# Optimization experiments

Hardware: AMD Instinct MI355X
Metric: run time of the kernel (lower is better)

Reference implementation:

```python
import jax, jax.numpy as jnp
import numpy as np

B, N, QD = 2, 2048, 1024
HEADS, DIM_HEAD = 16, 64
INNER = HEADS * DIM_HEAD  # 1024
SCALE = DIM_HEAD ** -0.5


def setup_inputs() -> dict:
    key = jax.random.key(0)
    ks = jax.random.split(key, 8)
    x = jax.random.normal(ks[0], (B, N, QD), dtype=jnp.float32)
    bias = jax.random.normal(ks[1], (B, N, N), dtype=jnp.float32)
    mask = jax.random.randint(ks[2], (B, N), 0, 2) > 0
    # parameters (nn.Linear stores weight [out, in]; we keep [in, out] and matmul x @ W)
    Wq = jax.random.normal(ks[3], (QD, INNER), dtype=jnp.float32) * (QD ** -0.5)
    Wkv = jax.random.normal(ks[4], (QD, 2 * INNER), dtype=jnp.float32) * (QD ** -0.5)
    Wo = jax.random.normal(ks[5], (INNER, QD), dtype=jnp.float32) * (INNER ** -0.5)
    bo = jax.random.normal(ks[6], (QD,), dtype=jnp.float32) * 0.01
    return {"x": x, "bias": bias, "mask": mask, "Wq": Wq, "Wkv": Wkv, "Wo": Wo, "bo": bo}


def reference(x, bias, mask, Wq, Wkv, Wo, bo):
    b, n, _ = x.shape
    q = x @ Wq                      # [b, n, inner]
    kv = x @ Wkv                    # [b, n, 2*inner] (context defaults to x)
    k, v = jnp.split(kv, 2, axis=-1)
    # split heads: [b, h, n, d]
    split = lambda t: t.reshape(b, n, HEADS, DIM_HEAD).transpose(0, 2, 1, 3)
    q, k, v = split(q), split(k), split(v)
    sim = jnp.einsum('bhid,bhjd->bhij', q, k) * SCALE   # [b, h, n, n]
    sim = sim + bias[:, None, :, :]                      # additive bias broadcast over heads
    max_neg = -jnp.finfo(sim.dtype).max
    sim = jnp.where(mask[:, None, None, :], sim, max_neg)  # per-key mask
    attn = jax.nn.softmax(sim, axis=-1)
    out = jnp.einsum('bhij,bhjd->bhid', attn, v)         # [b, h, n, d]
    out = out.transpose(0, 2, 1, 3).reshape(b, n, INNER)  # merge heads
    return out @ Wo + bo
```

## Files before the change

kernel.cpp:

```cpp
#include <hip/hip_runtime.h>
#include <hip/hip_bf16.h>
#include <stdint.h>

#define B_     2
#define N_     2048
#define QD_    1024
#define H_     16
#define DH_    64
#define INNER_ 1024
#define SCALE_ 0.125f

typedef unsigned short u16;
typedef __attribute__((ext_vector_type(8))) short bf16x8;
typedef __attribute__((ext_vector_type(4))) float f32x4;
typedef __attribute__((ext_vector_type(4))) unsigned short u16x4;
typedef __attribute__((ext_vector_type(8))) unsigned short u16x8;

__device__ inline u16 f2bf(float f) {
    union { float f; uint32_t u; } c; c.f = f;
    uint32_t r = c.u + 0x7FFFu + ((c.u >> 16) & 1u);
    return (u16)(r >> 16);
}
__device__ inline float bf2f(u16 s) {
    union { uint32_t u; float f; } c; c.u = ((uint32_t)s) << 16;
    return c.f;
}
__device__ inline void split2(float v, u16 &h, u16 &l) {
    u16 hs = f2bf(v);
    h = hs;
    l = f2bf(v - bf2f(hs));
}
__device__ inline unsigned pk2(float a, float b) {
    float2 f; f.x = a; f.y = b;
    union { __hip_bfloat162 v; unsigned u; } c;
    c.v = __float22bfloat162_rn(f);
    return c.u;
}

__global__ __launch_bounds__(256) void prep_kernel(
    const float* __restrict__ x, u16* __restrict__ xh, u16* __restrict__ xl,
    const float* __restrict__ Wq, const float* __restrict__ Wkv, const float* __restrict__ Wo,
    u16* __restrict__ wTh, u16* __restrict__ wTl,
    u16* __restrict__ woTh, u16* __restrict__ woTl)
{
    __shared__ float t[32][33];
    const int blk = blockIdx.x, tid = threadIdx.x;
    if (blk < 4096) {
        int idx = blk * 256 + tid;
        float4 v = ((const float4*)x)[idx];
        u16x4 hv, lv; u16 h, l;
        split2(v.x, h, l); hv.x = h; lv.x = l;
        split2(v.y, h, l); hv.y = h; lv.y = l;
        split2(v.z, h, l); hv.z = h; lv.z = l;
        split2(v.w, h, l); hv.w = h; lv.w = l;
        ((u16x4*)xh)[idx] = hv;
        ((u16x4*)xl)[idx] = lv;
        return;
    }
    int local = blk - 4096;
    const float* src; u16 *dhi, *dlo; int C, bx, by;
    if (local < 1024)      { src = Wq;  dhi = wTh;                dlo = wTl;                C = 1024; by = local >> 5; bx = local & 31; }
    else if (local < 3072) { int l2 = local - 1024; src = Wkv; dhi = wTh + 1024 * 1024; dlo = wTl + 1024 * 1024; C = 2048; by = l2 >> 6; bx = l2 & 63; }
    else                   { int l2 = local - 3072; src = Wo;  dhi = woTh;               dlo = woTl;               C = 1024; by = l2 >> 5; bx = l2 & 31; }
    const int x0 = bx * 32, y0 = by * 32;
    const int tx = tid & 31, ty = tid >> 5;
    for (int yy = ty; yy < 32; yy += 8)
        t[yy][tx] = src[(size_t)(y0 + yy) * C + x0 + tx];
    __syncthreads();
    for (int i = ty; i < 32; i += 8) {
        float v = t[tx][i];
        u16 h, l; split2(v, h, l);
        size_t o = (size_t)(x0 + i) * 1024 + y0 + tx;
        dhi[o] = h; dlo[o] = l;
    }
}

__global__ __launch_bounds__(256) void gemm_qkv_bias(
    int mode,
    const u16* __restrict__ Ah, const u16* __restrict__ Al,
    const u16* __restrict__ Bh,
    u16* __restrict__ qh,
    u16* __restrict__ kb, u16* __restrict__ vT,
    const float* __restrict__ bias, const int* __restrict__ mask,
    u16* __restrict__ bsw)
{
    __shared__ __align__(16) char smem[24576];
    const int tid = threadIdx.x;

    int gid = -1, bid = -1;
    if (mode == 1) {
        if (blockIdx.x < 768) gid = blockIdx.x; else bid = blockIdx.x - 768;
    } else if (mode == 0) gid = blockIdx.x;
    else bid = blockIdx.x;

    if (bid >= 0) {
        float (*t)[65] = (float(*)[65])smem;
        const int b = bid >> 10, rest = bid & 1023;
        const int k0 = (rest & 31) * 64, q0 = (rest >> 5) * 64;
#pragma unroll
        for (int it = 0; it < 16; it++) {
            int idx = it * 256 + tid;
            int qq = idx >> 6, kk = idx & 63;
            t[qq][kk] = bias[((size_t)b * N_ + q0 + qq) * N_ + k0 + kk];
        }
        __syncthreads();
        const u16 NEG = f2bf(-1e30f);
        const int qt = q0 >> 6, jt = k0 >> 7, w0 = (k0 >> 5) & 3;
        const int p = tid >> 1, hf = tid & 1;
        const int wv = w0 + (p >> 6), lane = p & 63;
        const int quad = lane >> 4, l16 = lane & 15;
        const int kbase = (p >> 6) * 32 + quad * 8 + hf * 4;
        const int4 mv = *(const int4*)&mask[b * N_ + k0 + kbase];
        const int mok[4] = { mv.x, mv.y, mv.z, mv.w };
        u16x8 o0, o1;
#pragma unroll
        for (int i = 0; i < 8; i++) {
            int m = i >> 2, r = i & 3;
            o0[i] = mok[r] ? f2bf(t[m * 16 + l16][kbase + r]) : NEG;
        }
#pragma unroll
        for (int i = 0; i < 8; i++) {
            int m = 2 + (i >> 2), r = i & 3;
            o1[i] = mok[r] ? f2bf(t[m * 16 + l16][kbase + r]) : NEG;
        }
        size_t ob = ((((size_t)b * 32 + qt) * 16 + jt) * 4 + wv) * 2048
                    + (size_t)lane * 32 + hf * 16;
        *(u16x8*)&bsw[ob]     = o0;
        *(u16x8*)&bsw[ob + 8] = o1;
        return;
    }

    u16* sAh = (u16*)smem;
    u16* sAl = (u16*)(smem + 8192);
    u16* sBh = (u16*)(smem + 16384);
    const int wave = tid >> 6, lane = tid & 63;
    const int quad = lane >> 4, l16 = lane & 15;
    const int wm = wave >> 1, wn = wave & 1;
    const int bx = gid % 24, by = gid / 24;
    const int bm = by * 128, bn = bx * 128;
    const bool comp = (bx < 8);

    f32x4 acc[4][4];
#pragma unroll
    for (int i = 0; i < 4; i++)
#pragma unroll
        for (int j = 0; j < 4; j++) acc[i][j] = (f32x4){0.f, 0.f, 0.f, 0.f};

    const int row0 = tid >> 2, g4 = tid & 3;
    const int r1 = row0, r2 = row0 + 64;
    const int gc1 = (g4 ^ (r1 & 3)) * 8, gc2 = (g4 ^ (r2 & 3)) * 8;
    const size_t a1 = (size_t)(bm + r1) * 1024 + gc1, a2 = (size_t)(bm + r2) * 1024 + gc2;
    const size_t b1 = (size_t)(bn + r1) * 1024 + gc1, b2 = (size_t)(bn + r2) * 1024 + gc2;
    const int w1 = r1 * 32 + g4 * 8, w2 = r2 * 32 + g4 * 8;

    bf16x8 pAh0, pAh1, pAl0, pAl1, pBh0, pBh1;
    pAh0 = *(const bf16x8*)&Ah[a1]; pAh1 = *(const bf16x8*)&Ah[a2];
    pBh0 = *(const bf16x8*)&Bh[b1]; pBh1 = *(const bf16x8*)&Bh[b2];
    if (comp) { pAl0 = *(const bf16x8*)&Al[a1]; pAl1 = *(const bf16x8*)&Al[a2]; }

    for (int k0 = 0; k0 < 1024; k0 += 32) {
        *(bf16x8*)&sAh[w1] = pAh0; *(bf16x8*)&sAh[w2] = pAh1;
        *(bf16x8*)&sBh[w1] = pBh0; *(bf16x8*)&sBh[w2] = pBh1;
        if (comp) { *(bf16x8*)&sAl[w1] = pAl0; *(bf16x8*)&sAl[w2] = pAl1; }
        __syncthreads();
        if (k0 + 32 < 1024) {
            int kn = k0 + 32;
            pAh0 = *(const bf16x8*)&Ah[a1 + kn]; pAh1 = *(const bf16x8*)&Ah[a2 + kn];
            pBh0 = *(const bf16x8*)&Bh[b1 + kn]; pBh1 = *(const bf16x8*)&Bh[b2 + kn];
            if (comp) { pAl0 = *(const bf16x8*)&Al[a1 + kn]; pAl1 = *(const bf16x8*)&Al[a2 + kn]; }
        }
        bf16x8 fah[4], fal[4], fbh[4];
#pragma unroll
        for (int s = 0; s < 4; s++) {
            int ra = wm * 64 + s * 16 + l16;
            int rb = wn * 64 + s * 16 + l16;
            int ca = (quad ^ (ra & 3)) * 8;
            int cb = (quad ^ (rb & 3)) * 8;
            fah[s] = *(const bf16x8*)&sAh[ra * 32 + ca];
            fbh[s] = *(const bf16x8*)&sBh[rb * 32 + cb];
            if (comp) fal[s] = *(const bf16x8*)&sAl[ra * 32 + ca];
        }
#pragma unroll
        for (int sm = 0; sm < 4; sm++)
#pragma unroll
            for (int sn = 0; sn < 4; sn++) {
                acc[sm][sn] = __builtin_amdgcn_mfma_f32_16x16x32_bf16(fah[sm], fbh[sn], acc[sm][sn], 0, 0, 0);
                if (comp)
                    acc[sm][sn] = __builtin_amdgcn_mfma_f32_16x16x32_bf16(fal[sm], fbh[sn], acc[sm][sn], 0, 0, 0);
            }
        __syncthreads();
    }
#pragma unroll
    for (int sm = 0; sm < 4; sm++) {
        int rowb = bm + wm * 64 + sm * 16 + quad * 4;
        int bb = rowb >> 11, i0 = rowb & 2047;
#pragma unroll
        for (int sn = 0; sn < 4; sn++) {
            int col = bn + wn * 64 + sn * 16 + l16;
            int region = col >> 10;
            int hh = (col >> 6) & 15;
            int d = col & 63;
            if (region == 0) {
#pragma unroll
                for (int r = 0; r < 4; r++) {
                    size_t o = (((size_t)(bb * H_ + hh)) * N_ + i0 + r) * DH_ + d;
                    qh[o] = f2bf(acc[sm][sn][r] * SCALE_);
                }
            } else if (region == 1) {
#pragma unroll
                for (int r = 0; r < 4; r++) {
                    size_t o = (((size_t)(bb * H_ + hh)) * N_ + i0 + r) * DH_ + d;
                    kb[o] = f2bf(acc[sm][sn][r]);
                }
            } else {
                u16x4 pv;
#pragma unroll
                for (int r = 0; r < 4; r++) pv[r] = f2bf(acc[sm][sn][r]);
                *(u16x4*)&vT[(((size_t)(bb * H_ + hh)) * DH_ + d) * N_ + i0] = pv;
            }
        }
    }
}

__global__ __launch_bounds__(256) void gemm_out(
    const u16* __restrict__ Ab,
    const u16* __restrict__ Bh,
    const float* __restrict__ bo, float* __restrict__ out)
{
    __shared__ __align__(16) u16 sA[128 * 32], sBh[64 * 32];
    const int tid = threadIdx.x;
    const int wave = tid >> 6, lane = tid & 63;
    const int quad = lane >> 4, l16 = lane & 15;
    const int wm = wave >> 1, wn = wave & 1;
    const int bm = blockIdx.y * 128, bn = blockIdx.x * 64;

    f32x4 acc[4][2];
#pragma unroll
    for (int i = 0; i < 4; i++)
#pragma unroll
        for (int j = 0; j < 2; j++) acc[i][j] = (f32x4){0.f, 0.f, 0.f, 0.f};

    const int row0 = tid >> 2, g4 = tid & 3;
    const int r1 = row0, r2 = row0 + 64;
    const int rb0 = tid >> 2;
    const int gc1 = (g4 ^ (r1 & 3)) * 8, gc2 = (g4 ^ (r2 & 3)) * 8;
    const size_t a1 = (size_t)(bm + r1) * 1024 + gc1, a2 = (size_t)(bm + r2) * 1024 + gc2;
    const size_t bgo = (size_t)(bn + rb0) * 1024 + gc1;
    const int w1 = r1 * 32 + g4 * 8, w2 = r2 * 32 + g4 * 8;
    const int wb = rb0 * 32 + g4 * 8;

    bf16x8 pA0, pA1, pBh0;
    pA0 = *(const bf16x8*)&Ab[a1]; pA1 = *(const bf16x8*)&Ab[a2];
    pBh0 = *(const bf16x8*)&Bh[bgo];

    for (int k0 = 0; k0 < 1024; k0 += 32) {
        *(bf16x8*)&sA[w1] = pA0;  *(bf16x8*)&sA[w2] = pA1;
        *(bf16x8*)&sBh[wb] = pBh0;
        __syncthreads();
        if (k0 + 32 < 1024) {
            int kn = k0 + 32;
            pA0 = *(const bf16x8*)&Ab[a1 + kn]; pA1 = *(const bf16x8*)&Ab[a2 + kn];
            pBh0 = *(const bf16x8*)&Bh[bgo + kn];
        }
        bf16x8 fa[4], fbh[2];
#pragma unroll
        for (int s = 0; s < 4; s++) {
            int ra = wm * 64 + s * 16 + l16;
            int ca = (quad ^ (ra & 3)) * 8;
            fa[s] = *(const bf16x8*)&sA[ra * 32 + ca];
        }
#pragma unroll
        for (int s = 0; s < 2; s++) {
            int rb = wn * 32 + s * 16 + l16;
            int cb = (quad ^ (rb & 3)) * 8;
            fbh[s] = *(const bf16x8*)&sBh[rb * 32 + cb];
        }
#pragma unroll
        for (int sm = 0; sm < 4; sm++)
#pragma unroll
            for (int sn = 0; sn < 2; sn++)
                acc[sm][sn] = __builtin_amdgcn_mfma_f32_16x16x32_bf16(fa[sm], fbh[sn], acc[sm][sn], 0, 0, 0);
        __syncthreads();
    }
#pragma unroll
    for (int sm = 0; sm < 4; sm++) {
        int rowb = bm + wm * 64 + sm * 16 + quad * 4;
#pragma unroll
        for (int sn = 0; sn < 2; sn++) {
            int col = bn + wn * 32 + sn * 16 + l16;
            float bv = bo[col];
#pragma unroll
            for (int r = 0; r < 4; r++)
                out[(size_t)(rowb + r) * 1024 + col] = acc[sm][sn][r] + bv;
        }
    }
}

#define LDK 72
#define LDV 128

__global__ __launch_bounds__(256, 2) void attn_kernel(
    const u16* __restrict__ qh,
    const u16* __restrict__ kb, const u16* __restrict__ vT,
    const u16* __restrict__ bsw, u16* __restrict__ ob)
{
    __shared__ __align__(16) char smem[35328];
    u16* sK  = (u16*)smem;
    u16* sVt = (u16*)(smem + 18432);
    float* rO = (float*)smem;
    float* rL = (float*)(smem + 34816);

    const int bh = blockIdx.y, b = bh >> 4, h = bh & 15;
    const int qt = blockIdx.x, qbase = qt * 64;
    const int tid = threadIdx.x, wave = tid >> 6, lane = tid & 63;
    const int quad = lane >> 4, l16 = lane & 15;

    bf16x8 aq[4][2];
#pragma unroll
    for (int m = 0; m < 4; m++) {
        size_t qo = ((size_t)bh * N_ + qbase + m * 16 + l16) * DH_ + quad * 8;
        aq[m][0] = *(const bf16x8*)&qh[qo];
        aq[m][1] = *(const bf16x8*)&qh[qo + 32];
    }
    f32x4 Oacc[4][4], lacc[4];
#pragma unroll
    for (int m = 0; m < 4; m++) {
        lacc[m] = (f32x4){0.f, 0.f, 0.f, 0.f};
#pragma unroll
        for (int nd = 0; nd < 4; nd++) Oacc[m][nd] = (f32x4){0.f, 0.f, 0.f, 0.f};
    }
    bf16x8 ones;
#pragma unroll
    for (int i = 0; i < 8; i++) ones[i] = (short)0x3F80;

    const int rK = tid >> 3, cK = (tid & 7) * 8;
    const int sigK = ((rK & 4) << 2) + ((rK >> 3) << 2) + (rK & 3);
    const int rV = tid >> 4;
    const int vg = tid & 15;
    const int cV = vg * 8;
    const int vsw = (vg ^ (rV & 7)) * 8;
    const int vrg = ((wave * 4 + quad) ^ (l16 & 7)) * 8;
    const size_t kgbase = (size_t)bh * N_ * DH_;
    const size_t vgbase = (size_t)bh * DH_ * N_;
    const size_t bswb = (size_t)(b * 32 + qt) * 131072 + (size_t)wave * 2048
                        + (size_t)lane * 32;

    bf16x8 pK[4], pV[4];
    u16x8 cB[4], nB[4];
#pragma unroll
    for (int it = 0; it < 4; it++) {
        pK[it] = *(const bf16x8*)&kb[kgbase + (size_t)(rK + it * 32) * DH_ + cK];
        pV[it] = *(const bf16x8*)&vT[vgbase + (size_t)(rV + it * 16) * N_ + cV];
    }
#pragma unroll
    for (int c = 0; c < 4; c++) cB[c] = *(const u16x8*)&bsw[bswb + c * 8];

    for (int jt = 0; jt < 16; jt++) {
#pragma unroll
        for (int it = 0; it < 4; it++) {
            *(bf16x8*)&sK[(it * 32 + sigK) * LDK + cK] = pK[it];
            *(bf16x8*)&sVt[(rV + it * 16) * LDV + vsw] = pV[it];
        }
        __syncthreads();
        {
            int jn = (jt + 1) & 15;
            int j0n = jn * 128;
#pragma unroll
            for (int it = 0; it < 4; it++) {
                pK[it] = *(const bf16x8*)&kb[kgbase + (size_t)(j0n + rK + it * 32) * DH_ + cK];
                pV[it] = *(const bf16x8*)&vT[vgbase + (size_t)(rV + it * 16) * N_ + j0n + cV];
            }
            size_t bb = bswb + (size_t)jn * 8192;
#pragma unroll
            for (int c = 0; c < 4; c++) nB[c] = *(const u16x8*)&bsw[bb + c * 8];
        }
        bf16x8 kf[2][2], vf[4];
#pragma unroll
        for (int n = 0; n < 2; n++)
#pragma unroll
            for (int s = 0; s < 2; s++)
                kf[n][s] = *(const bf16x8*)&sK[(wave * 32 + n * 16 + l16) * LDK + s * 32 + quad * 8];
#pragma unroll
        for (int nd = 0; nd < 4; nd++)
            vf[nd] = *(const bf16x8*)&sVt[(nd * 16 + l16) * LDV + vrg];

#pragma unroll
        for (int m = 0; m < 4; m++) {
            f32x4 S0 = (f32x4){0.f, 0.f, 0.f, 0.f};
            f32x4 S1 = (f32x4){0.f, 0.f, 0.f, 0.f};
#pragma unroll
            for (int s = 0; s < 2; s++) {
                S0 = __builtin_amdgcn_mfma_f32_16x16x32_bf16(kf[0][s], aq[m][s], S0, 0, 0, 0);
                S1 = __builtin_amdgcn_mfma_f32_16x16x32_bf16(kf[1][s], aq[m][s], S1, 0, 0, 0);
            }
            float p0[4], p1[4];
#pragma unroll
            for (int r = 0; r < 4; r++) {
                p0[r] = __expf(S0[r] + bf2f(cB[m >> 1][(m & 1) * 4 + r]));
                p1[r] = __expf(S1[r] + bf2f(cB[2 + (m >> 1)][(m & 1) * 4 + r]));
            }
            union { bf16x8 v; unsigned w[4]; } pa;
            pa.w[0] = pk2(p0[0], p0[1]);
            pa.w[1] = pk2(p0[2], p0[3]);
            pa.w[2] = pk2(p1[0], p1[1]);
            pa.w[3] = pk2(p1[2], p1[3]);
            lacc[m] = __builtin_amdgcn_mfma_f32_16x16x32_bf16(pa.v, ones, lacc[m], 0, 0, 0);
#pragma unroll
            for (int nd = 0; nd < 4; nd++)
                Oacc[m][nd] = __builtin_amdgcn_mfma_f32_16x16x32_bf16(pa.v, vf[nd], Oacc[m][nd], 0, 0, 0);
        }
#pragma unroll
        for (int c = 0; c < 4; c++) cB[c] = nB[c];
        __syncthreads();
    }

    if (wave >= 2) {
        int slot = wave - 2;
#pragma unroll
        for (int m = 0; m < 4; m++) {
#pragma unroll
            for (int nd = 0; nd < 4; nd++)
#pragma unroll
                for (int r = 0; r < 4; r++)
                    rO[(slot * 64 + m * 16 + quad * 4 + r) * 68 + nd * 16 + l16] = Oacc[m][nd][r];
            if (l16 == 0)
#pragma unroll
                for (int r = 0; r < 4; r++)
                    rL[slot * 64 + m * 16 + quad * 4 + r] = lacc[m][r];
        }
    }
    __syncthreads();
    if (wave < 2) {
        int slot = wave;
#pragma unroll
        for (int m = 0; m < 4; m++) {
#pragma unroll
            for (int nd = 0; nd < 4; nd++)
#pragma unroll
                for (int r = 0; r < 4; r++) {
                    int idx = (slot * 64 + m * 16 + quad * 4 + r) * 68 + nd * 16 + l16;
                    rO[idx] += Oacc[m][nd][r];
                }
            if (l16 == 0)
#pragma unroll
                for (int r = 0; r < 4; r++)
                    rL[slot * 64 + m * 16 + quad * 4 + r] += lacc[m][r];
        }
    }
    __syncthreads();
    {
        const int q = tid >> 2, dg = (tid & 3) * 16;
        float l = rL[q] + rL[64 + q];
        float inv = 1.f / l;
        f32x4 s[4];
#pragma unroll
        for (int i4 = 0; i4 < 4; i4++) {
            s[i4] = *(const f32x4*)&rO[(size_t)q * 68 + dg + i4 * 4];
            f32x4 v = *(const f32x4*)&rO[(size_t)(64 + q) * 68 + dg + i4 * 4];
            s[i4] += v;
        }
        size_t obase = ((size_t)b * N_ + qbase + q) * INNER_ + h * 64 + dg;
#pragma unroll
        for (int i4 = 0; i4 < 4; i4++) {
            u16x4 o4;
#pragma unroll
            for (int r = 0; r < 4; r++) o4[r] = f2bf(s[i4][r] * inv);
            *(u16x4*)&ob[obase + i4 * 4] = o4;
        }
    }
}

extern "C" void kernel_launch(void* const* d_in, const int* in_sizes, int n_in,
                              void* d_out, int out_size, void* d_ws, size_t ws_size,
                              hipStream_t stream)
{
    const float* x    = (const float*)d_in[0];
    const float* bias = (const float*)d_in[1];
    const int*   mask = (const int*)d_in[2];
    const float* Wq   = (const float*)d_in[3];
    const float* Wkv  = (const float*)d_in[4];
    const float* Wo   = (const float*)d_in[5];
    const float* bo   = (const float*)d_in[6];
    float* out = (float*)d_out;

    char* w = (char*)d_ws;
    const size_t MB = 1024 * 1024;
    u16* q_h   = (u16*)(w);
    u16* k_b   = (u16*)(w + 16 * MB);
    u16* v_T   = (u16*)(w + 24 * MB);
    u16* xs_h  = (u16*)(w + 32 * MB);
    u16* xs_l  = (u16*)(w + 40 * MB);
    u16* wT_h  = (u16*)(w + 48 * MB);
    u16* wT_l  = (u16*)(w + 54 * MB);
    u16* woT_h = (u16*)(w + 60 * MB);
    u16* woT_l = (u16*)(w + 62 * MB);
    u16* o_b   = (u16*)(w + 64 * MB);

    const size_t bsw_bytes = (size_t)2 * N_ * N_ * sizeof(u16);
    const bool concurrent = ws_size >= 72 * MB + bsw_bytes;

    prep_kernel<<<8192, 256, 0, stream>>>(x, xs_h, xs_l, Wq, Wkv, Wo, wT_h, wT_l, woT_h, woT_l);

    if (concurrent) {
        u16* bsw = (u16*)(w + 72 * MB);
        gemm_qkv_bias<<<2816, 256, 0, stream>>>(1, xs_h, xs_l, wT_h,
                                                q_h, k_b, v_T, bias, mask, bsw);
        attn_kernel<<<dim3(32, 32), 256, 0, stream>>>(q_h, k_b, v_T, bsw, o_b);
    } else {
        u16* bsw = (u16*)(w + 32 * MB);
        gemm_qkv_bias<<<768, 256, 0, stream>>>(0, xs_h, xs_l, wT_h,
                                               q_h, k_b, v_T, bias, mask, bsw);
        gemm_qkv_bias<<<2048, 256, 0, stream>>>(2, xs_h, xs_l, wT_h,
                                                q_h, k_b, v_T, bsw ? bias : bias, mask, bsw);
        attn_kernel<<<dim3(32, 32), 256, 0, stream>>>(q_h, k_b, v_T, bsw, o_b);
    }
    gemm_out<<<dim3(16, 32), 256, 0, stream>>>(o_b, woT_h, bo, out);
}
```

Before: 256.9 us.

## Use direct global-to-LDS loads with double-buffered tiles in projection GEMMs

Replaces the register-staged global→LDS copy in the QKV and output GEMMs with global_load_lds 16-byte async loads into a double-buffered shared-memory tile, dropping one barrier per k-step. This removes register pressure and VGPR round-trips for staging and lets the next tile load overlap the MFMA work. It doubles LDS usage (48KB in the QKV kernel), which can lower occupancy, and relies on the per-wave LDS layout matching the swizzled read pattern.

```diff
diff --git a/kernel.cpp b/kernel.cpp
--- a/kernel.cpp
+++ b/kernel.cpp
@@ -15,6 +15,10 @@
 typedef __attribute__((ext_vector_type(4))) float f32x4;
 typedef __attribute__((ext_vector_type(4))) unsigned short u16x4;
 typedef __attribute__((ext_vector_type(8))) unsigned short u16x8;
+
+#define GLD16(gp, lp) __builtin_amdgcn_global_load_lds( \
+    (const __attribute__((address_space(1))) unsigned int*)(gp), \
+    (__attribute__((address_space(3))) unsigned int*)(lp), 16, 0, 0)
 
 __device__ inline u16 f2bf(float f) {
     union { float f; uint32_t u; } c; c.f = f;
@@ -84,7 +88,7 @@
     const float* __restrict__ bias, const int* __restrict__ mask,
     u16* __restrict__ bsw)
 {
-    __shared__ __align__(16) char smem[24576];
+    __shared__ __align__(16) char smem[49152];
     const int tid = threadIdx.x;
 
     int gid = -1, bid = -1;
@@ -130,9 +134,6 @@
         return;
     }
 
-    u16* sAh = (u16*)smem;
-    u16* sAl = (u16*)(smem + 8192);
-    u16* sBh = (u16*)(smem + 16384);
     const int wave = tid >> 6, lane = tid & 63;
     const int quad = lane >> 4, l16 = lane & 15;
     const int wm = wave >> 1, wn = wave & 1;
@@ -151,24 +152,28 @@
     const int gc1 = (g4 ^ (r1 & 3)) * 8, gc2 = (g4 ^ (r2 & 3)) * 8;
     const size_t a1 = (size_t)(bm + r1) * 1024 + gc1, a2 = (size_t)(bm + r2) * 1024 + gc2;
     const size_t b1 = (size_t)(bn + r1) * 1024 + gc1, b2 = (size_t)(bn + r2) * 1024 + gc2;
-    const int w1 = r1 * 32 + g4 * 8, w2 = r2 * 32 + g4 * 8;
-
-    bf16x8 pAh0, pAh1, pAl0, pAl1, pBh0, pBh1;
-    pAh0 = *(const bf16x8*)&Ah[a1]; pAh1 = *(const bf16x8*)&Ah[a2];
-    pBh0 = *(const bf16x8*)&Bh[b1]; pBh1 = *(const bf16x8*)&Bh[b2];
-    if (comp) { pAl0 = *(const bf16x8*)&Al[a1]; pAl1 = *(const bf16x8*)&Al[a2]; }
-
+    const int ldsw = wave * 1024;
+
+    auto issue = [&](char* base, int kn) {
+        GLD16(Ah + a1 + kn, base + ldsw);
+        GLD16(Ah + a2 + kn, base + 4096 + ldsw);
+        GLD16(Bh + b1 + kn, base + 16384 + ldsw);
+        GLD16(Bh + b2 + kn, base + 20480 + ldsw);
+        if (comp) {
+            GLD16(Al + a1 + kn, base + 8192 + ldsw);
+            GLD16(Al + a2 + kn, base + 12288 + ldsw);
+        }
+    };
+
+    issue(smem, 0);
+    int cur = 0;
     for (int k0 = 0; k0 < 1024; k0 += 32) {
-        *(bf16x8*)&sAh[w1] = pAh0; *(bf16x8*)&sAh[w2] = pAh1;
-        *(bf16x8*)&sBh[w1] = pBh0; *(bf16x8*)&sBh[w2] = pBh1;
-        if (comp) { *(bf16x8*)&sAl[w1] = pAl0; *(bf16x8*)&sAl[w2] = pAl1; }
         __syncthreads();
-        if (k0 + 32 < 1024) {
-            int kn = k0 + 32;
-            pAh0 = *(const bf16x8*)&Ah[a1 + kn]; pAh1 = *(const bf16x8*)&Ah[a2 + kn];
-            pBh0 = *(const bf16x8*)&Bh[b1 + kn]; pBh1 = *(const bf16x8*)&Bh[b2 + kn];
-            if (comp) { pAl0 = *(const bf16x8*)&Al[a1 + kn]; pAl1 = *(const bf16x8*)&Al[a2 + kn]; }
-        }
+        char* cb_ = smem + cur * 24576;
+        if (k0 + 32 < 1024) issue(smem + (cur ^ 1) * 24576, k0 + 32);
+        const u16* cAh = (const u16*)cb_;
+        const u16* cAl = (const u16*)(cb_ + 8192);
+        const u16* cBh = (const u16*)(cb_ + 16384);
         bf16x8 fah[4], fal[4], fbh[4];
 #pragma unroll
         for (int s = 0; s < 4; s++) {
@@ -176,9 +181,9 @@
             int rb = wn * 64 + s * 16 + l16;
             int ca = (quad ^ (ra & 3)) * 8;
             int cb = (quad ^ (rb & 3)) * 8;
-            fah[s] = *(const bf16x8*)&sAh[ra * 32 + ca];
-            fbh[s] = *(const bf16x8*)&sBh[rb * 32 + cb];
-            if (comp) fal[s] = *(const bf16x8*)&sAl[ra * 32 + ca];
+            fah[s] = *(const bf16x8*)&cAh[ra * 32 + ca];
+            fbh[s] = *(const bf16x8*)&cBh[rb * 32 + cb];
+            if (comp) fal[s] = *(const bf16x8*)&cAl[ra * 32 + ca];
         }
 #pragma unroll
         for (int sm = 0; sm < 4; sm++)
@@ -188,7 +193,7 @@
                 if (comp)
                     acc[sm][sn] = __builtin_amdgcn_mfma_f32_16x16x32_bf16(fal[sm], fbh[sn], acc[sm][sn], 0, 0, 0);
             }
-        __syncthreads();
+        cur ^= 1;
     }
 #pragma unroll
     for (int sm = 0; sm < 4; sm++) {
@@ -227,7 +232,7 @@
     const u16* __restrict__ Bh,
     const float* __restrict__ bo, float* __restrict__ out)
 {
-    __shared__ __align__(16) u16 sA[128 * 32], sBh[64 * 32];
+    __shared__ __align__(16) char smem[24576];
     const int tid = threadIdx.x;
     const int wave = tid >> 6, lane = tid & 63;
     const int quad = lane >> 4, l16 = lane & 15;
@@ -242,45 +247,44 @@
 
     const int row0 = tid >> 2, g4 = tid & 3;
     const int r1 = row0, r2 = row0 + 64;
-    const int rb0 = tid >> 2;
     const int gc1 = (g4 ^ (r1 & 3)) * 8, gc2 = (g4 ^ (r2 & 3)) * 8;
     const size_t a1 = (size_t)(bm + r1) * 1024 + gc1, a2 = (size_t)(bm + r2) * 1024 + gc2;
-    const size_t bgo = (size_t)(bn + rb0) * 1024 + gc1;
-    const int w1 = r1 * 32 + g4 * 8, w2 = r2 * 32 + g4 * 8;
-    const int wb = rb0 * 32 + g4 * 8;
-
-    bf16x8 pA0, pA1, pBh0;
-    pA0 = *(const bf16x8*)&Ab[a1]; pA1 = *(const bf16x8*)&Ab[a2];
-    pBh0 = *(const bf16x8*)&Bh[bgo];
-
+    const size_t bgo = (size_t)(bn + r1) * 1024 + gc1;
+    const int ldsw = wave * 1024;
+
+    auto issue = [&](char* base, int kn) {
+        GLD16(Ab + a1 + kn, base + ldsw);
+        GLD16(Ab + a2 + kn, base + 4096 + ldsw);
+        GLD16(Bh + bgo + kn, base + 8192 + ldsw);
+    };
+
+    issue(smem, 0);
+    int cur = 0;
     for (int k0 = 0; k0 < 1024; k0 += 32) {
-        *(bf16x8*)&sA[w1] = pA0;  *(bf16x8*)&sA[w2] = pA1;
-        *(bf16x8*)&sBh[wb] = pBh0;
         __syncthreads();
-        if (k0 + 32 < 1024) {
-            int kn = k0 + 32;
-            pA0 = *(const bf16x8*)&Ab[a1 + kn]; pA1 = *(const bf16x8*)&Ab[a2 + kn];
-            pBh0 = *(const bf16x8*)&Bh[bgo + kn];
-        }
+        char* cb_ = smem + cur * 12288;
+        if (k0 + 32 < 1024) issue(smem + (cur ^ 1) * 12288, k0 + 32);
+        const u16* cA  = (const u16*)cb_;
+        const u16* cBh = (const u16*)(cb_ + 8192);
         bf16x8 fa[4], fbh[2];
 #pragma unroll
         for (int s = 0; s < 4; s++) {
             int ra = wm * 64 + s * 16 + l16;
             int ca = (quad ^ (ra & 3)) * 8;
-            fa[s] = *(const bf16x8*)&sA[ra * 32 + ca];
+            fa[s] = *(const bf16x8*)&cA[ra * 32 + ca];
         }
 #pragma unroll
         for (int s = 0; s < 2; s++) {
             int rb = wn * 32 + s * 16 + l16;
             int cb = (quad ^ (rb & 3)) * 8;
-            fbh[s] = *(const bf16x8*)&sBh[rb * 32 + cb];
+            fbh[s] = *(const bf16x8*)&cBh[rb * 32 + cb];
         }
 #pragma unroll
         for (int sm = 0; sm < 4; sm++)
 #pragma unroll
             for (int sn = 0; sn < 2; sn++)
                 acc[sm][sn] = __builtin_amdgcn_mfma_f32_16x16x32_bf16(fa[sm], fbh[sn], acc[sm][sn], 0, 0, 0);
-        __syncthreads();
+        cur ^= 1;
     }
 #pragma unroll
     for (int sm = 0; sm < 4; sm++) {
@@ -511,7 +515,7 @@
         gemm_qkv_bias<<<768, 256, 0, stream>>>(0, xs_h, xs_l, wT_h,
                                                q_h, k_b, v_T, bias, mask, bsw);
         gemm_qkv_bias<<<2048, 256, 0, stream>>>(2, xs_h, xs_l, wT_h,
-                                                q_h, k_b, v_T, bsw ? bias : bias, mask, bsw);
+                                                q_h, k_b, v_T, bias, mask, bsw);
         attn_kernel<<<dim3(32, 32), 256, 0, stream>>>(q_h, k_b, v_T, bsw, o_b);
     }
     gemm_out<<<dim3(16, 32), 256, 0, stream>>>(o_b, woT_h, bo, out);
```

New measurement: 251.0 us. -2.3%, faster.
